# Kernel optimization log

Hardware: AMD Instinct MI355X
Metric: run time of the kernel (lower is better)

## Reference

```python
import jax, jax.numpy as jnp
import numpy as np

# nuScenes-scale config: batch 2, 360x360 BEV grid (1440/4), 128 channels,
# 10 classes, 200 proposals, 3x3 NMS kernel, 40k occupied voxels per sample.
B, H, W_GRID, NUM_CLS, NUM_PROP, NMS_K = 2, 360, 360, 10, 200, 3
C = 128
N_PER_B = 40000
NEG_FILL = -1000000.0  # scatter_nd fill value from to_dense()


def _bev_pos():
    # replicates create_2D_grid: coord = (x_index_along_dim1, y_index_along_dim0)
    xs = jnp.arange(H, dtype=jnp.float32)
    ys = jnp.arange(W_GRID, dtype=jnp.float32)
    by, bx = jnp.meshgrid(xs, ys, indexing='ij')  # by[i,j]=i, bx[i,j]=j
    return jnp.stack([bx, by], axis=-1).reshape(-1, 2)  # [H*W, 2]


def setup_inputs() -> dict:
    key = jax.random.key(0)
    ks = jax.random.split(key, 10)
    # unique spatial locations per batch sample (sparse voxel coords)
    flats = [jax.random.permutation(ks[i], H * W_GRID)[:N_PER_B] for i in range(B)]
    flat = jnp.concatenate(flats)
    b = jnp.repeat(jnp.arange(B), N_PER_B)
    indices = jnp.stack([b, flat // W_GRID, flat % W_GRID], axis=1).astype(jnp.int32)
    features = jax.random.normal(ks[4], (B * N_PER_B, C), jnp.float32)
    # heatmap head (pointwise linears standing in for the submconv stack)
    W_hm1 = jax.random.normal(ks[5], (C, C), jnp.float32) * (2.0 / C) ** 0.5
    b_hm1 = jnp.zeros((C,), jnp.float32)
    W_hm2 = jax.random.normal(ks[6], (C, NUM_CLS), jnp.float32) * (2.0 / C) ** 0.5
    b_hm2 = jnp.full((NUM_CLS,), -2.19, jnp.float32)  # fc[-1].bias.fill_(-2.19)
    # class_encoding: nn.Conv1d(num_class, channels, 1)
    W_cls = jax.random.normal(ks[7], (C, NUM_CLS), jnp.float32) * 0.1
    b_cls = jnp.zeros((C,), jnp.float32)
    return dict(features=features, W_hm1=W_hm1, b_hm1=b_hm1, W_hm2=W_hm2,
                b_hm2=b_hm2, W_cls=W_cls, b_cls=b_cls, indices=indices)


def reference(features, W_hm1, b_hm1, W_hm2, b_hm2, W_cls, b_cls, indices):
    bidx, yi, xi = indices[:, 0], indices[:, 1], indices[:, 2]
    HW = H * W_GRID

    # --- x.dense(): scatter voxel features to dense BEV grid (zero fill) ---
    xd = jnp.zeros((B, H, W_GRID, C), features.dtype).at[bidx, yi, xi].set(features)
    x_flat = xd.reshape(B, HW, C).transpose(0, 2, 1)  # [B, C, HW]

    # --- heatmap head (per-voxel) then to_dense() with -1e6 fill ---
    hm = jax.nn.relu(features @ W_hm1 + b_hm1) @ W_hm2 + b_hm2  # [N, NUM_CLS]
    dense_hm = jnp.full((B, H, W_GRID, NUM_CLS), NEG_FILL, hm.dtype)
    dense_hm = dense_hm.at[bidx, yi, xi].set(hm).transpose(0, 3, 1, 2)  # [B,K,H,W]

    heat = jax.nn.sigmoid(dense_hm)  # detached in original

    # --- NMS-kernel peak extraction ---
    pad = NMS_K // 2
    inner = jax.lax.reduce_window(heat, -jnp.inf, jax.lax.max,
                                  (1, 1, NMS_K, NMS_K), (1, 1, 1, 1), 'VALID')
    local_max = jnp.zeros_like(heat).at[:, :, pad:H - pad, pad:W_GRID - pad].set(inner)
    # pedestrian (8) and traffic_cone (9): kernel size 1
    local_max = local_max.at[:, 8].set(heat[:, 8]).at[:, 9].set(heat[:, 9])
    heat = heat * (heat == local_max)
    heat_f = heat.reshape(B, NUM_CLS, HW)

    # --- top-k proposals over (class, location) ---
    _, top = jax.lax.top_k(heat_f.reshape(B, -1), NUM_PROP)  # [B, P]
    cls = top // HW
    idx = top % HW

    # --- gather proposal features + class encoding ---
    qf = jnp.take_along_axis(x_flat, jnp.broadcast_to(idx[:, None, :], (B, C, NUM_PROP)), axis=2)
    onehot = jax.nn.one_hot(cls, NUM_CLS, dtype=qf.dtype)  # [B, P, K]
    qf = qf + jnp.einsum('ck,bpk->bcp', W_cls, onehot) + b_cls[None, :, None]

    # --- proposal positions and heatmap scores ---
    query_pos = _bev_pos()[idx]  # [B, P, 2]
    qhs = jnp.take_along_axis(heat_f, jnp.broadcast_to(idx[:, None, :], (B, NUM_CLS, NUM_PROP)), axis=2)
    return qf, query_pos, qhs, cls
```

## Files before the change

### kernel.cpp

```cpp
#include <hip/hip_runtime.h>

#define HW 129600
#define WG 360
#define HG 360
#define NCLS 10
#define NPROP 200
#define CDIM 128
#define NROWS 80000
#define NB 2
#define NPB (NROWS / NB)
#define SEL_CAP 4096
#define HBINS 4096
#define RPB 64
#define PSTR 12
#define BPB 32

__device__ __align__(16) const float ZROW[12] = {0.f, 0.f, 0.f, 0.f, 0.f, 0.f,
                                                 0.f, 0.f, 0.f, 0.f, 0.f, 0.f};

__device__ __forceinline__ void lds_cp16(float* l, const float* g) {
  __builtin_amdgcn_global_load_lds(
      (const __attribute__((address_space(1))) void*)g,
      (__attribute__((address_space(3))) void*)l, 16, 0, 0);
}

__device__ __forceinline__ float4 fmax4(float4 a, float4 b) {
  float4 r;
  r.x = fmaxf(a.x, b.x);
  r.y = fmaxf(a.y, b.y);
  r.z = fmaxf(a.z, b.z);
  r.w = fmaxf(a.w, b.w);
  return r;
}

__global__ __launch_bounds__(256, 4) void k_head(
    const float* __restrict__ feat, const float* __restrict__ W1,
    const float* __restrict__ b1, const float* __restrict__ W2,
    const float* __restrict__ b2, const int* __restrict__ idxs,
    float* __restrict__ val_raw, int* __restrict__ rowmap,
    unsigned int* __restrict__ hist, int* __restrict__ sel_cnt) {
  __shared__ __align__(16) float lds_w[2][16 * 128];
  __shared__ __align__(16) float lds_f[2][RPB * 16];
  const int tid = threadIdx.x;
  const int row0 = blockIdx.x * RPB;
  const int tc = tid & 31;
  const int tr = tid >> 5;
  const int wv = tid >> 6;
  const int lane = tid & 63;

  auto stage = [&](int kt, int nb) {
#pragma unroll
    for (int c = 0; c < 2; ++c) {
      const int off = (wv * 2 + c) * 256;
      lds_cp16(&lds_w[nb][off], W1 + kt * 2048 + off + lane * 4);
    }
    {
      const int off = wv * 256;
      const int fidx = off + lane * 4;
      const int r = fidx >> 4, kk = fidx & 15;
      lds_cp16(&lds_f[nb][off],
               feat + (size_t)(row0 + r) * CDIM + kt * 16 + kk);
    }
  };

  stage(0, 0);
  if (blockIdx.x == 0) {
    uint4* h4 = (uint4*)hist;
    for (int i = tid; i < (NB * HBINS) / 4; i += 256)
      h4[i] = make_uint4(0u, 0u, 0u, 0u);
    if (tid < 2) sel_cnt[tid] = 0;
  }
  if (tid < RPB) {
    int row = row0 + tid;
    int bb = idxs[row * 3 + 0];
    int yy = idxs[row * 3 + 1];
    int xx = idxs[row * 3 + 2];
    rowmap[(size_t)bb * HW + yy * WG + xx] = row;
  }
  __syncthreads();

  float acc[8][4];
#pragma unroll
  for (int r = 0; r < 8; ++r)
#pragma unroll
    for (int c = 0; c < 4; ++c) acc[r][c] = 0.f;

  for (int kt = 0; kt < 8; ++kt) {
    const int cb = kt & 1;
    if (kt < 7) stage(kt + 1, cb ^ 1);
#pragma unroll
    for (int kg = 0; kg < 4; ++kg) {
      float4 w0 = *(const float4*)(&lds_w[cb][(kg * 4 + 0) * 128 + tc * 4]);
      float4 w1 = *(const float4*)(&lds_w[cb][(kg * 4 + 1) * 128 + tc * 4]);
      float4 w2 = *(const float4*)(&lds_w[cb][(kg * 4 + 2) * 128 + tc * 4]);
      float4 w3 = *(const float4*)(&lds_w[cb][(kg * 4 + 3) * 128 + tc * 4]);
#pragma unroll
      for (int r = 0; r < 8; ++r) {
        float4 fv = *(const float4*)(&lds_f[cb][(tr * 8 + r) * 16 + kg * 4]);
        acc[r][0] = fmaf(fv.x, w0.x, acc[r][0]);
        acc[r][0] = fmaf(fv.y, w1.x, acc[r][0]);
        acc[r][0] = fmaf(fv.z, w2.x, acc[r][0]);
        acc[r][0] = fmaf(fv.w, w3.x, acc[r][0]);
        acc[r][1] = fmaf(fv.x, w0.y, acc[r][1]);
        acc[r][1] = fmaf(fv.y, w1.y, acc[r][1]);
        acc[r][1] = fmaf(fv.z, w2.y, acc[r][1]);
        acc[r][1] = fmaf(fv.w, w3.y, acc[r][1]);
        acc[r][2] = fmaf(fv.x, w0.z, acc[r][2]);
        acc[r][2] = fmaf(fv.y, w1.z, acc[r][2]);
        acc[r][2] = fmaf(fv.z, w2.z, acc[r][2]);
        acc[r][2] = fmaf(fv.w, w3.z, acc[r][2]);
        acc[r][3] = fmaf(fv.x, w0.w, acc[r][3]);
        acc[r][3] = fmaf(fv.y, w1.w, acc[r][3]);
        acc[r][3] = fmaf(fv.z, w2.w, acc[r][3]);
        acc[r][3] = fmaf(fv.w, w3.w, acc[r][3]);
      }
    }
    __syncthreads();
  }

  float* w2t = &lds_f[0][0];
  for (int i = tid; i < CDIM * NCLS; i += 256) {
    int k = i / NCLS, j = i - k * NCLS;
    w2t[j * 128 + k] = W2[i];
  }
  __syncthreads();

  float* hbuf = &lds_w[0][0];
  float4 b1v = *(const float4*)(b1 + tc * 4);
#pragma unroll
  for (int half = 0; half < 2; ++half) {
    if ((tr >> 2) == half) {
      int ltr = tr & 3;
#pragma unroll
      for (int r = 0; r < 8; ++r) {
        float4 h;
        h.x = fmaxf(acc[r][0] + b1v.x, 0.f);
        h.y = fmaxf(acc[r][1] + b1v.y, 0.f);
        h.z = fmaxf(acc[r][2] + b1v.z, 0.f);
        h.w = fmaxf(acc[r][3] + b1v.w, 0.f);
        *(float4*)(hbuf + (ltr * 8 + r) * 128 + tc * 4) = h;
      }
    }
    __syncthreads();
    for (int o = tid; o < 32 * NCLS; o += 256) {
      int r = o / NCLS, j = o - r * NCLS;
      float s = b2[j];
      for (int i4 = 0; i4 < 32; ++i4) {
        int k4 = (i4 + tid) & 31;
        float4 hv = *(const float4*)(hbuf + r * 128 + k4 * 4);
        float4 wv2 = *(const float4*)(w2t + j * 128 + k4 * 4);
        s = fmaf(hv.x, wv2.x, s);
        s = fmaf(hv.y, wv2.y, s);
        s = fmaf(hv.z, wv2.z, s);
        s = fmaf(hv.w, wv2.w, s);
      }
      float heat = 1.0f / (1.0f + expf(-s));
      int gr = half * 32 + r;
      val_raw[(size_t)(row0 + gr) * PSTR + j] = heat;
    }
    __syncthreads();
  }
}

__global__ __launch_bounds__(256) void k_hist(
    const float* __restrict__ val_raw, const int* __restrict__ idxs,
    const int* __restrict__ rowmap, float* __restrict__ val,
    unsigned int* __restrict__ hist) {
  __shared__ unsigned int lh[HBINS];
  const int tid = threadIdx.x;
  const int row = blockIdx.x * 256 + tid;
  const int blk_b = (blockIdx.x * 256 >= NPB) ? 1 : 0;
  for (int i = tid; i < HBINS; i += 256) lh[i] = 0;
  __syncthreads();

  float v[10];
  int bb = 0;
  const bool valid = row < NROWS;
  if (valid) {
    bb = (row >= NPB) ? 1 : 0;
    const int y = idxs[row * 3 + 1];
    const int x = idxs[row * 3 + 2];
    const int pos = y * WG + x;
    const float* cbase = val_raw + (size_t)row * PSTR;
    float4 c0 = *(const float4*)(cbase + 0);
    float4 c1 = *(const float4*)(cbase + 4);
    float2 c89 = *(const float2*)(cbase + 8);
    const bool interior = (y > 0 && y < HG - 1 && x > 0 && x < WG - 1);
    if (interior) {
      const int dyA[8] = {0, 0, -1, -1, -1, 1, 1, 1};
      const int dxA[8] = {-1, 1, -1, 0, 1, -1, 0, 1};
      float4 m0 = c0, m1 = c1;
      const int* rmb = rowmap + (size_t)bb * HW + pos;
#pragma unroll
      for (int n = 0; n < 8; ++n) {
        const int nrow = rmb[dyA[n] * WG + dxA[n]];
        bool ok =
            ((unsigned)nrow < NROWS) && ((nrow >= NPB) == (bb == 1));
        if (ok) {
          ok = (idxs[nrow * 3 + 1] == y + dyA[n]) &&
               (idxs[nrow * 3 + 2] == x + dxA[n]);
        }
        const float* p = ok ? (val_raw + (size_t)nrow * PSTR) : ZROW;
        m0 = fmax4(m0, *(const float4*)(p + 0));
        m1 = fmax4(m1, *(const float4*)(p + 4));
      }
      v[0] = (c0.x == m0.x) ? c0.x : 0.f;
      v[1] = (c0.y == m0.y) ? c0.y : 0.f;
      v[2] = (c0.z == m0.z) ? c0.z : 0.f;
      v[3] = (c0.w == m0.w) ? c0.w : 0.f;
      v[4] = (c1.x == m1.x) ? c1.x : 0.f;
      v[5] = (c1.y == m1.y) ? c1.y : 0.f;
      v[6] = (c1.z == m1.z) ? c1.z : 0.f;
      v[7] = (c1.w == m1.w) ? c1.w : 0.f;
    } else {
      v[0] = v[1] = v[2] = v[3] = v[4] = v[5] = v[6] = v[7] = 0.f;
    }
    v[8] = c89.x;
    v[9] = c89.y;
    float4 s0 = {v[0], v[1], v[2], v[3]};
    float4 s1 = {v[4], v[5], v[6], v[7]};
    float4 s2 = {v[8], v[9], 0.f, 0.f};
    *(float4*)(val + (size_t)row * PSTR + 0) = s0;
    *(float4*)(val + (size_t)row * PSTR + 4) = s1;
    *(float4*)(val + (size_t)row * PSTR + 8) = s2;
#pragma unroll
    for (int c = 0; c < 10; ++c) {
      if (v[c] > 0.f) {
        unsigned int bin = __float_as_uint(v[c]) >> 18;
        if (bb == blk_b)
          atomicAdd(&lh[bin], 1u);
        else
          atomicAdd(&hist[(size_t)bb * HBINS + bin], 1u);
      }
    }
  }
  __syncthreads();
  unsigned int* gh = hist + (size_t)blk_b * HBINS;
  for (int i = tid; i < HBINS; i += 256) {
    unsigned int c = lh[i];
    if (c) atomicAdd(&gh[i], c);
  }
}

__global__ __launch_bounds__(256) void k_collect(
    const float* __restrict__ val, const int* __restrict__ idxs,
    const unsigned int* __restrict__ hist, unsigned long long* __restrict__ sel,
    int* __restrict__ sel_cnt) {
  __shared__ unsigned int coarse[256];
  __shared__ unsigned int fine16[16];
  __shared__ int sT[2];
  __shared__ int sCi[2];
  const int tid = threadIdx.x;
  for (int bb = 0; bb < NB; ++bb) {
    const unsigned int* h = hist + (size_t)bb * HBINS;
    const uint4* h4 = (const uint4*)(h + tid * 16);
    unsigned int s = 0;
#pragma unroll
    for (int i = 0; i < 4; ++i) {
      uint4 q = h4[i];
      s += q.x + q.y + q.z + q.w;
    }
    if (tid == 0) {
      sCi[bb] = -1;
      sT[bb] = 0;
    }
    coarse[tid] = s;
    __syncthreads();
#pragma unroll
    for (int off = 1; off < 256; off <<= 1) {
      unsigned int vv = (tid + off < 256) ? coarse[tid + off] : 0u;
      __syncthreads();
      coarse[tid] += vv;
      __syncthreads();
    }
    if (coarse[tid] >= NPROP) atomicMax(&sCi[bb], tid);
    __syncthreads();
    const int ci = sCi[bb];
    if (ci >= 0) {
      if (tid < 16) fine16[tid] = h[ci * 16 + tid];
      __syncthreads();
      if (tid == 0) {
        unsigned int cum = (ci + 1 < 256) ? coarse[ci + 1] : 0u;
        int t = 15;
        for (; t > 0; --t) {
          unsigned int c = fine16[t];
          if (cum + c >= NPROP) break;
          cum += c;
        }
        sT[bb] = ci * 16 + t;
      }
    }
    __syncthreads();
  }
  const int row = blockIdx.x * 256 + tid;
  const bool valid = row < NROWS;
  const int bb = (valid && row >= NPB) ? 1 : 0;
  const int T = sT[bb];
  float v[12];
  int pos = 0;
  if (valid) {
    *(float4*)(v + 0) = *(const float4*)(val + (size_t)row * PSTR + 0);
    *(float4*)(v + 4) = *(const float4*)(val + (size_t)row * PSTR + 4);
    *(float4*)(v + 8) = *(const float4*)(val + (size_t)row * PSTR + 8);
    pos = idxs[row * 3 + 1] * WG + idxs[row * 3 + 2];
  }
  const int lane = tid & 63;
#pragma unroll
  for (int cl = 0; cl < 10; ++cl) {
    float vv = valid ? v[cl] : 0.f;
    unsigned int bits = __float_as_uint(vv);
    bool pred = (vv > 0.f) && ((int)(bits >> 18) >= T);
    unsigned long long m0 = __ballot(pred && (bb == 0));
    unsigned long long m1 = __ballot(pred && (bb == 1));
    if (pred) {
      unsigned long long mask = bb ? m1 : m0;
      int leader = __ffsll((unsigned long long)mask) - 1;
      int lb = __popcll(mask & ((1ull << lane) - 1ull));
      int base = 0;
      if (lane == leader) base = atomicAdd(&sel_cnt[bb], (int)__popcll(mask));
      base = __shfl(base, leader, 64);
      unsigned int gidx = (unsigned int)cl * HW + (unsigned int)pos;
      unsigned long long key =
          ((unsigned long long)bits << 32) | (unsigned long long)(~gidx);
      int slot = base + lb;
      if (slot < SEL_CAP) sel[(size_t)bb * SEL_CAP + slot] = key;
    }
  }
}

__global__ __launch_bounds__(256) void k_final(
    const unsigned long long* __restrict__ sel, const int* __restrict__ sel_cnt,
    const float* __restrict__ val, const int* __restrict__ rowmap,
    const float* __restrict__ feat, const float* __restrict__ Wc,
    const float* __restrict__ bc, float* __restrict__ out) {
  __shared__ unsigned long long sk[SEL_CAP];
  __shared__ unsigned long long winners[NPROP];
  __shared__ int wcls[NPROP];
  __shared__ int wrow[NPROP];
  const int b = blockIdx.x / BPB;
  const int part = blockIdx.x % BPB;
  const int tid = threadIdx.x;
  int M = sel_cnt[b];
  if (M > SEL_CAP) M = SEL_CAP;
  for (int i = tid; i < M; i += 256) sk[i] = sel[(size_t)b * SEL_CAP + i];
  __syncthreads();
  for (int i = tid; i < M; i += 256) {
    unsigned long long key = sk[i];
    int rank = 0;
    for (int j = 0; j < M; ++j) rank += (sk[j] > key) ? 1 : 0;
    if (rank < NPROP) winners[rank] = key;
  }
  __syncthreads();
  if (tid < NPROP) {
    unsigned long long key = winners[tid];
    unsigned int gidx = ~((unsigned int)(key & 0xFFFFFFFFull));
    int cls = (int)(gidx / HW);
    int pos = (int)(gidx - (unsigned int)cls * HW);
    wcls[tid] = cls;
    wrow[tid] = rowmap[(size_t)b * HW + pos];
    if (part == 0) {
      int y = pos / WG, x = pos - y * WG;
      out[51200 + ((size_t)b * NPROP + tid) * 2 + 0] = (float)x;
      out[51200 + ((size_t)b * NPROP + tid) * 2 + 1] = (float)y;
      out[56000 + b * NPROP + tid] = (float)cls;
    }
  }
  __syncthreads();
  for (int o = part * 256 + tid; o < NCLS * NPROP; o += BPB * 256) {
    int j = o / NPROP, pp = o - j * NPROP;
    out[52000 + (size_t)b * NCLS * NPROP + o] = val[(size_t)wrow[pp] * PSTR + j];
  }
  for (int o = part * 256 + tid; o < CDIM * NPROP; o += BPB * 256) {
    int c = o / NPROP, pp = o - c * NPROP;
    out[(size_t)b * CDIM * NPROP + o] =
        feat[(size_t)wrow[pp] * CDIM + c] + Wc[c * NCLS + wcls[pp]] + bc[c];
  }
}

extern "C" void kernel_launch(void* const* d_in, const int* in_sizes, int n_in,
                              void* d_out, int out_size, void* d_ws,
                              size_t ws_size, hipStream_t stream) {
  const float* feat = (const float*)d_in[0];
  const float* W1 = (const float*)d_in[1];
  const float* b1 = (const float*)d_in[2];
  const float* W2 = (const float*)d_in[3];
  const float* b2 = (const float*)d_in[4];
  const float* Wc = (const float*)d_in[5];
  const float* bc = (const float*)d_in[6];
  const int* idxs = (const int*)d_in[7];
  float* out = (float*)d_out;

  char* ws = (char*)d_ws;
  unsigned int* hist = (unsigned int*)(ws + 0);
  int* rowmap = (int*)(ws + 32768);
  unsigned long long* sel = (unsigned long long*)(ws + 1069568);
  int* sel_cnt = (int*)(ws + 1135104);
  float* val_raw = (float*)(ws + 1135120);
  float* val = (float*)(ws + 4975120);

  k_head<<<NROWS / RPB, 256, 0, stream>>>(feat, W1, b1, W2, b2, idxs, val_raw,
                                          rowmap, hist, sel_cnt);
  k_hist<<<(NROWS + 255) / 256, 256, 0, stream>>>(val_raw, idxs, rowmap, val,
                                                  hist);
  k_collect<<<(NROWS + 255) / 256, 256, 0, stream>>>(val, idxs, hist, sel,
                                                     sel_cnt);
  k_final<<<NB * BPB, 256, 0, stream>>>(sel, sel_cnt, val, rowmap, feat, Wc, bc,
                                        out);
}
```

Before: 180.5 us.

## Fuse hist, collect and final kernels into one cooperative kernel with grid syncs

Replaces three separate kernel launches (NMS+histogram, threshold collect, final top-k/gather) with one cooperative kernel of 256 blocks that uses grid.sync between phases. NMS results are held in registers across the first grid barrier, so the collect phase no longer re-reads val. Per-block shared histograms now cover both batches, which removes the global atomics for rows from the other batch. The cost is two grid-wide barriers, a cooperative launch, and more rows per block, which may lower parallelism during the NMS phase.

```diff
diff --git a/kernel.cpp b/kernel.cpp
--- a/kernel.cpp
+++ b/kernel.cpp
@@ -1,4 +1,7 @@
 #include <hip/hip_runtime.h>
+#include <hip/hip_cooperative_groups.h>
+
+namespace cg = cooperative_groups;
 
 #define HW 129600
 #define WG 360
@@ -14,6 +17,9 @@
 #define RPB 64
 #define PSTR 12
 #define BPB 32
+#define TGRID 256
+#define CHUNK ((NROWS + TGRID - 1) / TGRID)
+#define NIT ((CHUNK + 255) / 256)
 
 __device__ __align__(16) const float ZROW[12] = {0.f, 0.f, 0.f, 0.f, 0.f, 0.f,
                                                  0.f, 0.f, 0.f, 0.f, 0.f, 0.f};
@@ -162,95 +168,111 @@
   }
 }
 
-__global__ __launch_bounds__(256) void k_hist(
+__global__ __launch_bounds__(256, 2) void k_tail(
     const float* __restrict__ val_raw, const int* __restrict__ idxs,
     const int* __restrict__ rowmap, float* __restrict__ val,
-    unsigned int* __restrict__ hist) {
-  __shared__ unsigned int lh[HBINS];
-  const int tid = threadIdx.x;
-  const int row = blockIdx.x * 256 + tid;
-  const int blk_b = (blockIdx.x * 256 >= NPB) ? 1 : 0;
-  for (int i = tid; i < HBINS; i += 256) lh[i] = 0;
-  __syncthreads();
-
-  float v[10];
-  int bb = 0;
-  const bool valid = row < NROWS;
-  if (valid) {
-    bb = (row >= NPB) ? 1 : 0;
-    const int y = idxs[row * 3 + 1];
-    const int x = idxs[row * 3 + 2];
-    const int pos = y * WG + x;
-    const float* cbase = val_raw + (size_t)row * PSTR;
-    float4 c0 = *(const float4*)(cbase + 0);
-    float4 c1 = *(const float4*)(cbase + 4);
-    float2 c89 = *(const float2*)(cbase + 8);
-    const bool interior = (y > 0 && y < HG - 1 && x > 0 && x < WG - 1);
-    if (interior) {
-      const int dyA[8] = {0, 0, -1, -1, -1, 1, 1, 1};
-      const int dxA[8] = {-1, 1, -1, 0, 1, -1, 0, 1};
-      float4 m0 = c0, m1 = c1;
-      const int* rmb = rowmap + (size_t)bb * HW + pos;
-#pragma unroll
-      for (int n = 0; n < 8; ++n) {
-        const int nrow = rmb[dyA[n] * WG + dxA[n]];
-        bool ok =
-            ((unsigned)nrow < NROWS) && ((nrow >= NPB) == (bb == 1));
-        if (ok) {
-          ok = (idxs[nrow * 3 + 1] == y + dyA[n]) &&
-               (idxs[nrow * 3 + 2] == x + dxA[n]);
-        }
-        const float* p = ok ? (val_raw + (size_t)nrow * PSTR) : ZROW;
-        m0 = fmax4(m0, *(const float4*)(p + 0));
-        m1 = fmax4(m1, *(const float4*)(p + 4));
-      }
-      v[0] = (c0.x == m0.x) ? c0.x : 0.f;
-      v[1] = (c0.y == m0.y) ? c0.y : 0.f;
-      v[2] = (c0.z == m0.z) ? c0.z : 0.f;
-      v[3] = (c0.w == m0.w) ? c0.w : 0.f;
-      v[4] = (c1.x == m1.x) ? c1.x : 0.f;
-      v[5] = (c1.y == m1.y) ? c1.y : 0.f;
-      v[6] = (c1.z == m1.z) ? c1.z : 0.f;
-      v[7] = (c1.w == m1.w) ? c1.w : 0.f;
-    } else {
-      v[0] = v[1] = v[2] = v[3] = v[4] = v[5] = v[6] = v[7] = 0.f;
-    }
-    v[8] = c89.x;
-    v[9] = c89.y;
-    float4 s0 = {v[0], v[1], v[2], v[3]};
-    float4 s1 = {v[4], v[5], v[6], v[7]};
-    float4 s2 = {v[8], v[9], 0.f, 0.f};
-    *(float4*)(val + (size_t)row * PSTR + 0) = s0;
-    *(float4*)(val + (size_t)row * PSTR + 4) = s1;
-    *(float4*)(val + (size_t)row * PSTR + 8) = s2;
-#pragma unroll
-    for (int c = 0; c < 10; ++c) {
-      if (v[c] > 0.f) {
-        unsigned int bin = __float_as_uint(v[c]) >> 18;
-        if (bb == blk_b)
-          atomicAdd(&lh[bin], 1u);
-        else
-          atomicAdd(&hist[(size_t)bb * HBINS + bin], 1u);
-      }
-    }
-  }
-  __syncthreads();
-  unsigned int* gh = hist + (size_t)blk_b * HBINS;
-  for (int i = tid; i < HBINS; i += 256) {
-    unsigned int c = lh[i];
-    if (c) atomicAdd(&gh[i], c);
-  }
-}
-
-__global__ __launch_bounds__(256) void k_collect(
-    const float* __restrict__ val, const int* __restrict__ idxs,
-    const unsigned int* __restrict__ hist, unsigned long long* __restrict__ sel,
-    int* __restrict__ sel_cnt) {
+    unsigned int* __restrict__ hist, unsigned long long* __restrict__ sel,
+    int* __restrict__ sel_cnt, const float* __restrict__ feat,
+    const float* __restrict__ Wc, const float* __restrict__ bc,
+    float* __restrict__ out) {
+  __shared__ __align__(16) unsigned int lhbuf[NB * HBINS];
+  __shared__ unsigned long long winners[NPROP];
+  __shared__ int wcls[NPROP];
+  __shared__ int wrow[NPROP];
   __shared__ unsigned int coarse[256];
   __shared__ unsigned int fine16[16];
-  __shared__ int sT[2];
-  __shared__ int sCi[2];
+  __shared__ int sT[NB];
+  __shared__ int sCi[NB];
+
+  cg::grid_group grid = cg::this_grid();
   const int tid = threadIdx.x;
+  const int blk = blockIdx.x;
+  const int r0 = blk * CHUNK;
+  const int rend = (r0 + CHUNK < NROWS) ? (r0 + CHUNK) : NROWS;
+
+  for (int i = tid; i < NB * HBINS; i += 256) lhbuf[i] = 0u;
+  __syncthreads();
+
+  float v2[NIT][10];
+  int pos2[NIT];
+  int bb2[NIT];
+
+#pragma unroll
+  for (int it = 0; it < NIT; ++it) {
+    const int row = r0 + it * 256 + tid;
+    const bool valid = row < rend;
+    float* v = v2[it];
+    if (valid) {
+      const int bb = (row >= NPB) ? 1 : 0;
+      bb2[it] = bb;
+      const int y = idxs[row * 3 + 1];
+      const int x = idxs[row * 3 + 2];
+      const int pos = y * WG + x;
+      pos2[it] = pos;
+      const float* cbase = val_raw + (size_t)row * PSTR;
+      float4 c0 = *(const float4*)(cbase + 0);
+      float4 c1 = *(const float4*)(cbase + 4);
+      float2 c89 = *(const float2*)(cbase + 8);
+      const bool interior = (y > 0 && y < HG - 1 && x > 0 && x < WG - 1);
+      if (interior) {
+        const int dyA[8] = {0, 0, -1, -1, -1, 1, 1, 1};
+        const int dxA[8] = {-1, 1, -1, 0, 1, -1, 0, 1};
+        float4 m0 = c0, m1 = c1;
+        const int* rmb = rowmap + (size_t)bb * HW + pos;
+#pragma unroll
+        for (int n = 0; n < 8; ++n) {
+          const int nrow = rmb[dyA[n] * WG + dxA[n]];
+          bool ok = ((unsigned)nrow < NROWS) && ((nrow >= NPB) == (bb == 1));
+          if (ok) {
+            ok = (idxs[nrow * 3 + 1] == y + dyA[n]) &&
+                 (idxs[nrow * 3 + 2] == x + dxA[n]);
+          }
+          const float* p = ok ? (val_raw + (size_t)nrow * PSTR) : ZROW;
+          m0 = fmax4(m0, *(const float4*)(p + 0));
+          m1 = fmax4(m1, *(const float4*)(p + 4));
+        }
+        v[0] = (c0.x == m0.x) ? c0.x : 0.f;
+        v[1] = (c0.y == m0.y) ? c0.y : 0.f;
+        v[2] = (c0.z == m0.z) ? c0.z : 0.f;
+        v[3] = (c0.w == m0.w) ? c0.w : 0.f;
+        v[4] = (c1.x == m1.x) ? c1.x : 0.f;
+        v[5] = (c1.y == m1.y) ? c1.y : 0.f;
+        v[6] = (c1.z == m1.z) ? c1.z : 0.f;
+        v[7] = (c1.w == m1.w) ? c1.w : 0.f;
+      } else {
+        v[0] = v[1] = v[2] = v[3] = v[4] = v[5] = v[6] = v[7] = 0.f;
+      }
+      v[8] = c89.x;
+      v[9] = c89.y;
+      float4 s0 = {v[0], v[1], v[2], v[3]};
+      float4 s1 = {v[4], v[5], v[6], v[7]};
+      float4 s2 = {v[8], v[9], 0.f, 0.f};
+      *(float4*)(val + (size_t)row * PSTR + 0) = s0;
+      *(float4*)(val + (size_t)row * PSTR + 4) = s1;
+      *(float4*)(val + (size_t)row * PSTR + 8) = s2;
+#pragma unroll
+      for (int c = 0; c < 10; ++c) {
+        if (v[c] > 0.f) {
+          unsigned int bin = __float_as_uint(v[c]) >> 18;
+          atomicAdd(&lhbuf[bb * HBINS + bin], 1u);
+        }
+      }
+    } else {
+      bb2[it] = 0;
+      pos2[it] = 0;
+#pragma unroll
+      for (int c = 0; c < 10; ++c) v[c] = 0.f;
+    }
+  }
+  __syncthreads();
+  for (int i = tid; i < NB * HBINS; i += 256) {
+    unsigned int c = lhbuf[i];
+    if (c) atomicAdd(&hist[i], c);
+  }
+
+  __threadfence();
+  grid.sync();
+
   for (int bb = 0; bb < NB; ++bb) {
     const unsigned int* h = hist + (size_t)bb * HBINS;
     const uint4* h4 = (const uint4*)(h + tid * 16);
@@ -292,54 +314,45 @@
     }
     __syncthreads();
   }
-  const int row = blockIdx.x * 256 + tid;
-  const bool valid = row < NROWS;
-  const int bb = (valid && row >= NPB) ? 1 : 0;
-  const int T = sT[bb];
-  float v[12];
-  int pos = 0;
-  if (valid) {
-    *(float4*)(v + 0) = *(const float4*)(val + (size_t)row * PSTR + 0);
-    *(float4*)(v + 4) = *(const float4*)(val + (size_t)row * PSTR + 4);
-    *(float4*)(v + 8) = *(const float4*)(val + (size_t)row * PSTR + 8);
-    pos = idxs[row * 3 + 1] * WG + idxs[row * 3 + 2];
-  }
+
   const int lane = tid & 63;
 #pragma unroll
-  for (int cl = 0; cl < 10; ++cl) {
-    float vv = valid ? v[cl] : 0.f;
-    unsigned int bits = __float_as_uint(vv);
-    bool pred = (vv > 0.f) && ((int)(bits >> 18) >= T);
-    unsigned long long m0 = __ballot(pred && (bb == 0));
-    unsigned long long m1 = __ballot(pred && (bb == 1));
-    if (pred) {
-      unsigned long long mask = bb ? m1 : m0;
-      int leader = __ffsll((unsigned long long)mask) - 1;
-      int lb = __popcll(mask & ((1ull << lane) - 1ull));
-      int base = 0;
-      if (lane == leader) base = atomicAdd(&sel_cnt[bb], (int)__popcll(mask));
-      base = __shfl(base, leader, 64);
-      unsigned int gidx = (unsigned int)cl * HW + (unsigned int)pos;
-      unsigned long long key =
-          ((unsigned long long)bits << 32) | (unsigned long long)(~gidx);
-      int slot = base + lb;
-      if (slot < SEL_CAP) sel[(size_t)bb * SEL_CAP + slot] = key;
-    }
-  }
-}
-
-__global__ __launch_bounds__(256) void k_final(
-    const unsigned long long* __restrict__ sel, const int* __restrict__ sel_cnt,
-    const float* __restrict__ val, const int* __restrict__ rowmap,
-    const float* __restrict__ feat, const float* __restrict__ Wc,
-    const float* __restrict__ bc, float* __restrict__ out) {
-  __shared__ unsigned long long sk[SEL_CAP];
-  __shared__ unsigned long long winners[NPROP];
-  __shared__ int wcls[NPROP];
-  __shared__ int wrow[NPROP];
-  const int b = blockIdx.x / BPB;
-  const int part = blockIdx.x % BPB;
-  const int tid = threadIdx.x;
+  for (int it = 0; it < NIT; ++it) {
+    const int row = r0 + it * 256 + tid;
+    const bool valid = row < rend;
+    const int bb = bb2[it];
+    const int T = sT[bb];
+    const int pos = pos2[it];
+#pragma unroll
+    for (int cl = 0; cl < 10; ++cl) {
+      float vv = valid ? v2[it][cl] : 0.f;
+      unsigned int bits = __float_as_uint(vv);
+      bool pred = (vv > 0.f) && ((int)(bits >> 18) >= T);
+      unsigned long long m0 = __ballot(pred && (bb == 0));
+      unsigned long long m1 = __ballot(pred && (bb == 1));
+      if (pred) {
+        unsigned long long mask = bb ? m1 : m0;
+        int leader = __ffsll((unsigned long long)mask) - 1;
+        int lb = __popcll(mask & ((1ull << lane) - 1ull));
+        int base = 0;
+        if (lane == leader) base = atomicAdd(&sel_cnt[bb], (int)__popcll(mask));
+        base = __shfl(base, leader, 64);
+        unsigned int gidx = (unsigned int)cl * HW + (unsigned int)pos;
+        unsigned long long key =
+            ((unsigned long long)bits << 32) | (unsigned long long)(~gidx);
+        int slot = base + lb;
+        if (slot < SEL_CAP) sel[(size_t)bb * SEL_CAP + slot] = key;
+      }
+    }
+  }
+
+  __threadfence();
+  grid.sync();
+
+  if (blk >= NB * BPB) return;
+  const int b = blk / BPB;
+  const int part = blk % BPB;
+  unsigned long long* sk = (unsigned long long*)lhbuf;
   int M = sel_cnt[b];
   if (M > SEL_CAP) M = SEL_CAP;
   for (int i = tid; i < M; i += 256) sk[i] = sel[(size_t)b * SEL_CAP + i];
@@ -400,10 +413,9 @@
 
   k_head<<<NROWS / RPB, 256, 0, stream>>>(feat, W1, b1, W2, b2, idxs, val_raw,
                                           rowmap, hist, sel_cnt);
-  k_hist<<<(NROWS + 255) / 256, 256, 0, stream>>>(val_raw, idxs, rowmap, val,
-                                                  hist);
-  k_collect<<<(NROWS + 255) / 256, 256, 0, stream>>>(val, idxs, hist, sel,
-                                                     sel_cnt);
-  k_final<<<NB * BPB, 256, 0, stream>>>(sel, sel_cnt, val, rowmap, feat, Wc, bc,
-                                        out);
+
+  void* args[] = {&val_raw, &idxs, &rowmap, &val,  &hist, &sel,
+                  &sel_cnt, &feat, &Wc,     &bc,   &out};
+  hipLaunchCooperativeKernel((void*)k_tail, dim3(TGRID), dim3(256), args, 0,
+                             stream);
 }
```

Result: slower. 280.5 us (+55.4%).

## Parallelize NMS neighbor lookup across 8 lanes per voxel with shuffle max

Applied to the files above, without the earlier changes.

The NMS/histogram kernel now gives each voxel 8 threads, one per 3x3 neighbour, instead of one thread looping over all 8 neighbours. Each lane gathers one neighbour's rowmap, index and heat values, and a 3-step xor-shuffle reduces to the neighbour maximum. The aim is to hide the serial chain of dependent gathers with more parallel memory requests. The LDS-privatized histogram is dropped in favour of direct global atomics, which cuts the LDS init and flush but may increase global atomic contention.

```diff
diff --git a/kernel.cpp b/kernel.cpp
--- a/kernel.cpp
+++ b/kernel.cpp
@@ -14,23 +14,12 @@
 #define RPB 64
 #define PSTR 12
 #define BPB 32
-
-__device__ __align__(16) const float ZROW[12] = {0.f, 0.f, 0.f, 0.f, 0.f, 0.f,
-                                                 0.f, 0.f, 0.f, 0.f, 0.f, 0.f};
+#define RPH 32
 
 __device__ __forceinline__ void lds_cp16(float* l, const float* g) {
   __builtin_amdgcn_global_load_lds(
       (const __attribute__((address_space(1))) void*)g,
       (__attribute__((address_space(3))) void*)l, 16, 0, 0);
-}
-
-__device__ __forceinline__ float4 fmax4(float4 a, float4 b) {
-  float4 r;
-  r.x = fmaxf(a.x, b.x);
-  r.y = fmaxf(a.y, b.y);
-  r.z = fmaxf(a.z, b.z);
-  r.w = fmaxf(a.w, b.w);
-  return r;
 }
 
 __global__ __launch_bounds__(256, 4) void k_head(
@@ -166,52 +155,57 @@
     const float* __restrict__ val_raw, const int* __restrict__ idxs,
     const int* __restrict__ rowmap, float* __restrict__ val,
     unsigned int* __restrict__ hist) {
-  __shared__ unsigned int lh[HBINS];
   const int tid = threadIdx.x;
-  const int row = blockIdx.x * 256 + tid;
-  const int blk_b = (blockIdx.x * 256 >= NPB) ? 1 : 0;
-  for (int i = tid; i < HBINS; i += 256) lh[i] = 0;
-  __syncthreads();
-
-  float v[10];
-  int bb = 0;
-  const bool valid = row < NROWS;
-  if (valid) {
-    bb = (row >= NPB) ? 1 : 0;
-    const int y = idxs[row * 3 + 1];
-    const int x = idxs[row * 3 + 2];
-    const int pos = y * WG + x;
+  const int g = tid >> 3;
+  const int n = tid & 7;
+  const int row = blockIdx.x * RPH + g;
+  const int bb = (row >= NPB) ? 1 : 0;
+  const int y = idxs[row * 3 + 1];
+  const int x = idxs[row * 3 + 2];
+  const int pos = y * WG + x;
+  const bool interior = (y > 0 && y < HG - 1 && x > 0 && x < WG - 1);
+  const int dy = (n < 2) ? 0 : ((n < 5) ? -1 : 1);
+  const int dx = (n < 2) ? (n * 2 - 1) : ((n < 5) ? (n - 3) : (n - 6));
+
+  int nrow = -1;
+  if (interior) nrow = rowmap[(size_t)bb * HW + pos + dy * WG + dx];
+  const bool inb = ((unsigned)nrow < NROWS) && ((nrow >= NPB) == (bb == 1));
+  const int safe = inb ? nrow : 0;
+  const int y2 = idxs[safe * 3 + 1];
+  const int x2 = idxs[safe * 3 + 2];
+  const bool ok = inb && (y2 == y + dy) && (x2 == x + dx);
+  float4 a = *(const float4*)(val_raw + (size_t)safe * PSTR);
+  float4 b = *(const float4*)(val_raw + (size_t)safe * PSTR + 4);
+  if (!ok) {
+    a.x = a.y = a.z = a.w = 0.f;
+    b.x = b.y = b.z = b.w = 0.f;
+  }
+#pragma unroll
+  for (int m = 1; m <= 4; m <<= 1) {
+    a.x = fmaxf(a.x, __shfl_xor(a.x, m));
+    a.y = fmaxf(a.y, __shfl_xor(a.y, m));
+    a.z = fmaxf(a.z, __shfl_xor(a.z, m));
+    a.w = fmaxf(a.w, __shfl_xor(a.w, m));
+    b.x = fmaxf(b.x, __shfl_xor(b.x, m));
+    b.y = fmaxf(b.y, __shfl_xor(b.y, m));
+    b.z = fmaxf(b.z, __shfl_xor(b.z, m));
+    b.w = fmaxf(b.w, __shfl_xor(b.w, m));
+  }
+  if (n == 0) {
     const float* cbase = val_raw + (size_t)row * PSTR;
     float4 c0 = *(const float4*)(cbase + 0);
     float4 c1 = *(const float4*)(cbase + 4);
     float2 c89 = *(const float2*)(cbase + 8);
-    const bool interior = (y > 0 && y < HG - 1 && x > 0 && x < WG - 1);
+    float v[10];
     if (interior) {
-      const int dyA[8] = {0, 0, -1, -1, -1, 1, 1, 1};
-      const int dxA[8] = {-1, 1, -1, 0, 1, -1, 0, 1};
-      float4 m0 = c0, m1 = c1;
-      const int* rmb = rowmap + (size_t)bb * HW + pos;
-#pragma unroll
-      for (int n = 0; n < 8; ++n) {
-        const int nrow = rmb[dyA[n] * WG + dxA[n]];
-        bool ok =
-            ((unsigned)nrow < NROWS) && ((nrow >= NPB) == (bb == 1));
-        if (ok) {
-          ok = (idxs[nrow * 3 + 1] == y + dyA[n]) &&
-               (idxs[nrow * 3 + 2] == x + dxA[n]);
-        }
-        const float* p = ok ? (val_raw + (size_t)nrow * PSTR) : ZROW;
-        m0 = fmax4(m0, *(const float4*)(p + 0));
-        m1 = fmax4(m1, *(const float4*)(p + 4));
-      }
-      v[0] = (c0.x == m0.x) ? c0.x : 0.f;
-      v[1] = (c0.y == m0.y) ? c0.y : 0.f;
-      v[2] = (c0.z == m0.z) ? c0.z : 0.f;
-      v[3] = (c0.w == m0.w) ? c0.w : 0.f;
-      v[4] = (c1.x == m1.x) ? c1.x : 0.f;
-      v[5] = (c1.y == m1.y) ? c1.y : 0.f;
-      v[6] = (c1.z == m1.z) ? c1.z : 0.f;
-      v[7] = (c1.w == m1.w) ? c1.w : 0.f;
+      v[0] = (c0.x >= a.x) ? c0.x : 0.f;
+      v[1] = (c0.y >= a.y) ? c0.y : 0.f;
+      v[2] = (c0.z >= a.z) ? c0.z : 0.f;
+      v[3] = (c0.w >= a.w) ? c0.w : 0.f;
+      v[4] = (c1.x >= b.x) ? c1.x : 0.f;
+      v[5] = (c1.y >= b.y) ? c1.y : 0.f;
+      v[6] = (c1.z >= b.z) ? c1.z : 0.f;
+      v[7] = (c1.w >= b.w) ? c1.w : 0.f;
     } else {
       v[0] = v[1] = v[2] = v[3] = v[4] = v[5] = v[6] = v[7] = 0.f;
     }
@@ -223,22 +217,11 @@
     *(float4*)(val + (size_t)row * PSTR + 0) = s0;
     *(float4*)(val + (size_t)row * PSTR + 4) = s1;
     *(float4*)(val + (size_t)row * PSTR + 8) = s2;
+    unsigned int* gh = hist + (size_t)bb * HBINS;
 #pragma unroll
     for (int c = 0; c < 10; ++c) {
-      if (v[c] > 0.f) {
-        unsigned int bin = __float_as_uint(v[c]) >> 18;
-        if (bb == blk_b)
-          atomicAdd(&lh[bin], 1u);
-        else
-          atomicAdd(&hist[(size_t)bb * HBINS + bin], 1u);
-      }
-    }
-  }
-  __syncthreads();
-  unsigned int* gh = hist + (size_t)blk_b * HBINS;
-  for (int i = tid; i < HBINS; i += 256) {
-    unsigned int c = lh[i];
-    if (c) atomicAdd(&gh[i], c);
+      if (v[c] > 0.f) atomicAdd(&gh[__float_as_uint(v[c]) >> 18], 1u);
+    }
   }
 }
 
@@ -400,8 +383,7 @@
 
   k_head<<<NROWS / RPB, 256, 0, stream>>>(feat, W1, b1, W2, b2, idxs, val_raw,
                                           rowmap, hist, sel_cnt);
-  k_hist<<<(NROWS + 255) / 256, 256, 0, stream>>>(val_raw, idxs, rowmap, val,
-                                                  hist);
+  k_hist<<<NROWS / RPH, 256, 0, stream>>>(val_raw, idxs, rowmap, val, hist);
   k_collect<<<(NROWS + 255) / 256, 256, 0, stream>>>(val, idxs, hist, sel,
                                                      sel_cnt);
   k_final<<<NB * BPB, 256, 0, stream>>>(sel, sel_cnt, val, rowmap, feat, Wc, bc,
```

Result: slower. 570.4 us (+216.0%).
